# Performance work log

Measured on AMD Instinct MI355X. Metric: run time of the kernel, lower is better.

Reference implementation:

```python
import jax, jax.numpy as jnp
import numpy as np


def setup_inputs() -> dict:
    key = jax.random.key(0)
    k1, k2, k3 = jax.random.split(key, 3)
    B, C, H, W = 4, 256, 96, 128
    F = 9
    return {
        "input1": jax.random.normal(k1, (B, C, H, W), dtype=jnp.float32),
        "input2": jax.random.normal(k2, (B, C, H, W), dtype=jnp.float32),
        "weights": jax.random.normal(k3, (C, F, F), dtype=jnp.float32),
        "filter_size": 9,
        "dilation": 2,
        "num_groups": 4,
    }


def _weighted_corr(input1, input2, weights, filter_size, dilation, num_groups):
    B, C, H, W = input1.shape
    F = filter_size
    G = num_groups
    Cg = C // G
    r = F // 2
    pad = r * dilation
    # zero-pad input2 spatially so out-of-bounds displacements contribute 0
    p2 = jnp.pad(input2, ((0, 0), (0, 0), (pad, pad), (pad, pad)))
    in1g = input1.reshape(B, G, Cg, H, W)
    outs = []  # one [B, G, H, W] map per window offset (dy, dx)
    for dy in range(F):
        for dx in range(F):
            shifted = p2[:, :, dy * dilation:dy * dilation + H,
                         dx * dilation:dx * dilation + W].reshape(B, G, Cg, H, W)
            wg = weights[:, dy, dx].reshape(G, Cg)
            outs.append(jnp.einsum('bgchw,bgchw,gc->bghw', in1g, shifted, wg))
    out = jnp.stack(outs, axis=2)  # [B, G, F*F, H, W]
    return out.reshape(B, G * F * F, H, W)


def reference(input1, input2, weights, filter_size, dilation, num_groups):
    return _weighted_corr(input1, input2, weights, filter_size, dilation, num_groups)
```

## Files before the change

### kernel.cpp

```cpp
#include <hip/hip_runtime.h>

#define B_   4
#define C_   256
#define H_   96
#define W_   128
#define F_   9
#define G_   4
#define CG   64
#define NC4  16
#define NO   81
#define TH   2
#define TCOLS (W_ + 16)
#define HW_  (H_ * W_)

#define NDY   3
#define PROWS (2 * NDY)
#define PTE   (PROWS * TCOLS)
#define PNK   4

typedef _Float16 half2v __attribute__((ext_vector_type(2)));
typedef unsigned u32x2 __attribute__((ext_vector_type(2)));

__device__ __forceinline__ half2v u2h(unsigned u) {
    half2v h; __builtin_memcpy(&h, &u, 4); return h;
}
__device__ __forceinline__ unsigned h2u(half2v h) {
    unsigned u; __builtin_memcpy(&u, &h, 4); return u;
}
__device__ __forceinline__ half2v pkrtz(float a, float b) {
    auto r = __builtin_amdgcn_cvt_pkrtz(a, b);
    half2v h; __builtin_memcpy(&h, &r, 4); return h;
}
__device__ __forceinline__ unsigned pkrtz_u(float a, float b) {
    auto r = __builtin_amdgcn_cvt_pkrtz(a, b);
    unsigned u; __builtin_memcpy(&u, &r, 4); return u;
}

#if __has_builtin(__builtin_amdgcn_fdot2)
#define FDOT2(a, b, c) __builtin_amdgcn_fdot2((a), (b), (c), false)
#else
__device__ __forceinline__ float fdot2_fb(half2v a, half2v b, float c) {
    return c + (float)a[0] * (float)b[0] + (float)a[1] * (float)b[1];
}
#define FDOT2(a, b, c) fdot2_fb((a), (b), (c))
#endif

__global__ void pack_weights_kernel(const float* __restrict__ w,
                                    u32x2* __restrict__ wp) {
    int i = blockIdx.x * blockDim.x + threadIdx.x;
    if (i >= G_ * NC4 * NO) return;
    int o  = i % NO;
    int c4 = (i / NO) % NC4;
    int g  = i / (NO * NC4);
    const float* base = w + (size_t)(g * CG + 4 * c4) * NO + o;
    u32x2 r;
    r.x = pkrtz_u(base[0], base[NO]);
    r.y = pkrtz_u(base[2 * NO], base[3 * NO]);
    wp[i] = r;
}

template <bool PACKED>
__global__ __launch_bounds__(256)
void wcorr_kernel(const float* __restrict__ in1, const float* __restrict__ in2,
                  const u32x2* __restrict__ wp, const float* __restrict__ wraw,
                  float* __restrict__ out) {
    __shared__ u32x2 tile[2][PTE];

    int bid  = blockIdx.x;
    int xcd  = bid & 7;
    int slot = bid >> 3;
    int pair = xcd + 8 * (slot / 144);
    int rem  = slot % 144;
    int pass = rem / 48;
    int hblk = rem % 48;
    int b = pair >> 2, g = pair & 3;
    int h0 = hblk * TH;

    int t  = threadIdx.x;
    int ty = t >> 7;
    int tx = t & 127;

    const float* in1g = in1 + (size_t)(b * C_ + g * CG) * HW_;
    const float* in2g = in2 + (size_t)(b * C_ + g * CG) * HW_;

    const int gr0 = h0 - 8 + 6 * pass;
    int po[PNK]; unsigned msk[PNK];
#pragma unroll
    for (int k = 0; k < PNK; ++k) {
        int pidx = k * 256 + t;
        int row  = pidx / TCOLS;
        int hcol = pidx - row * TCOLS;
        int gr = gr0 + row, gc = hcol - 8;
        bool inb = (pidx < PTE) && gr >= 0 && gr < H_ && gc >= 0 && gc < W_;
        int off = gr * W_ + gc;
        off = off < 0 ? 0 : (off > HW_ - 1 ? HW_ - 1 : off);
        po[k]  = off;
        float m = inb ? 1.f : 0.f;
        msk[k] = pkrtz_u(m, m);
    }

    float acc[NDY * F_];
#pragma unroll
    for (int o = 0; o < NDY * F_; ++o) acc[o] = 0.f;

    float sv0[PNK], sv1[PNK], sv2[PNK], sv3[PNK];

    auto LOADS = [&](int c4n) {
        const float* chb = in2g + (size_t)(4 * c4n) * HW_;
#pragma unroll
        for (int k = 0; k < PNK; ++k) {
            const float* q = chb + po[k];
            sv0[k] = q[0];        sv1[k] = q[HW_];
            sv2[k] = q[2 * HW_];  sv3[k] = q[3 * HW_];
        }
    };
    auto WRITE = [&](u32x2* dst) {
#pragma unroll
        for (int k = 0; k < PNK; ++k) {
            if (k < PNK - 1 || t < PTE - (PNK - 1) * 256) {
                half2v m = u2h(msk[k]);
                u32x2 r;
                r.x = h2u(u2h(pkrtz_u(sv0[k], sv1[k])) * m);
                r.y = h2u(u2h(pkrtz_u(sv2[k], sv3[k])) * m);
                dst[k * 256 + t] = r;
            }
        }
    };

    LOADS(0);
    WRITE(tile[0]);
    LOADS(1);

    const int in1off = (h0 + ty) * W_ + tx;
    float a0 = in1g[in1off], a1 = in1g[in1off + HW_];
    float a2 = in1g[in1off + 2 * HW_], a3 = in1g[in1off + 3 * HW_];

    const int lbase = ty * TCOLS + tx;

    for (int c4 = 0; c4 < NC4; ++c4) {
        __syncthreads();

        if (c4 + 1 < NC4) WRITE(tile[(c4 + 1) & 1]);
        if (c4 + 2 < NC4) LOADS(c4 + 2);

        const u32x2* lt = tile[c4 & 1];
        half2v ha = pkrtz(a0, a1);
        half2v hb = pkrtz(a2, a3);
        if (c4 + 1 < NC4) {
            const float* pp = in1g + (size_t)(4 * (c4 + 1)) * HW_ + in1off;
            a0 = pp[0]; a1 = pp[HW_]; a2 = pp[2 * HW_]; a3 = pp[3 * HW_];
        }

        const u32x2* wrow = PACKED ? (wp + ((size_t)g * NC4 + c4) * NO + pass * NDY * F_) : nullptr;
        const float* wr = wraw + (size_t)(g * CG + 4 * c4) * NO + pass * NDY * F_;

#pragma unroll
        for (int dyp = 0; dyp < NDY; ++dyp) {
#pragma unroll
            for (int dx = 0; dx < F_; ++dx) {
                const int oo = dyp * F_ + dx;
                u32x2 uv = lt[lbase + dyp * 2 * TCOLS + dx * 2];
                half2v wa, wb;
                if (PACKED) {
                    u32x2 wv = wrow[oo];
                    wa = u2h(wv.x); wb = u2h(wv.y);
                } else {
                    wa = pkrtz(wr[oo], wr[oo + NO]);
                    wb = pkrtz(wr[oo + 2 * NO], wr[oo + 3 * NO]);
                }
                half2v p0 = wa * ha;
                half2v p1 = wb * hb;
                float s = FDOT2(p0, u2h(uv.x), acc[oo]);
                acc[oo]  = FDOT2(p1, u2h(uv.y), s);
            }
        }
    }

    size_t obase = (((size_t)pair * NO + pass * NDY * F_) * H_ + (h0 + ty)) * W_ + tx;
#pragma unroll
    for (int oo = 0; oo < NDY * F_; ++oo)
        out[obase + (size_t)oo * HW_] = acc[oo];
}

extern "C" void kernel_launch(void* const* d_in, const int* in_sizes, int n_in,
                              void* d_out, int out_size, void* d_ws, size_t ws_size,
                              hipStream_t stream) {
    const float* in1  = (const float*)d_in[0];
    const float* in2  = (const float*)d_in[1];
    const float* wraw = (const float*)d_in[2];
    float* out = (float*)d_out;

    const size_t wp_bytes = (size_t)G_ * NC4 * NO * 8;
    const int nblocks = 16 * 3 * (H_ / TH);

    if (ws_size >= wp_bytes) {
        u32x2* wp = (u32x2*)d_ws;
        int n = G_ * NC4 * NO;
        pack_weights_kernel<<<(n + 255) / 256, 256, 0, stream>>>(wraw, wp);
        wcorr_kernel<true><<<nblocks, 256, 0, stream>>>(in1, in2, wp, wraw, out);
    } else {
        wcorr_kernel<false><<<nblocks, 256, 0, stream>>>(in1, in2, nullptr, wraw, out);
    }
}
```

Baseline: 76.82 us.

## Switch to 4x64 spatial tiles and 8-channel half-packed LDS slabs

```diff
diff --git a/kernel.cpp b/kernel.cpp
--- a/kernel.cpp
+++ b/kernel.cpp
@@ -7,19 +7,18 @@
 #define F_   9
 #define G_   4
 #define CG   64
-#define NC4  16
+#define NC8  8
 #define NO   81
-#define TH   2
-#define TCOLS (W_ + 16)
 #define HW_  (H_ * W_)
 
 #define NDY   3
-#define PROWS (2 * NDY)
-#define PTE   (PROWS * TCOLS)
-#define PNK   4
+#define TROWS 8
+#define TCOLS 80
+#define PTE   (TROWS * TCOLS)
+#define PNK   3
 
 typedef _Float16 half2v __attribute__((ext_vector_type(2)));
-typedef unsigned u32x2 __attribute__((ext_vector_type(2)));
+typedef unsigned u32x4 __attribute__((ext_vector_type(4)));
 
 __device__ __forceinline__ half2v u2h(unsigned u) {
     half2v h; __builtin_memcpy(&h, &u, 4); return h;
@@ -46,25 +45,27 @@
 #endif
 
 __global__ void pack_weights_kernel(const float* __restrict__ w,
-                                    u32x2* __restrict__ wp) {
+                                    u32x4* __restrict__ wp) {
     int i = blockIdx.x * blockDim.x + threadIdx.x;
-    if (i >= G_ * NC4 * NO) return;
+    if (i >= G_ * NC8 * NO) return;
     int o  = i % NO;
-    int c4 = (i / NO) % NC4;
-    int g  = i / (NO * NC4);
-    const float* base = w + (size_t)(g * CG + 4 * c4) * NO + o;
-    u32x2 r;
-    r.x = pkrtz_u(base[0], base[NO]);
+    int c8 = (i / NO) % NC8;
+    int g  = i / (NO * NC8);
+    const float* base = w + (size_t)(g * CG + 8 * c8) * NO + o;
+    u32x4 r;
+    r.x = pkrtz_u(base[0 * NO], base[1 * NO]);
     r.y = pkrtz_u(base[2 * NO], base[3 * NO]);
+    r.z = pkrtz_u(base[4 * NO], base[5 * NO]);
+    r.w = pkrtz_u(base[6 * NO], base[7 * NO]);
     wp[i] = r;
 }
 
 template <bool PACKED>
 __global__ __launch_bounds__(256)
 void wcorr_kernel(const float* __restrict__ in1, const float* __restrict__ in2,
-                  const u32x2* __restrict__ wp, const float* __restrict__ wraw,
+                  const u32x4* __restrict__ wp, const float* __restrict__ wraw,
                   float* __restrict__ out) {
-    __shared__ u32x2 tile[2][PTE];
+    __shared__ u32x4 tile[2][PTE];
 
     int bid  = blockIdx.x;
     int xcd  = bid & 7;
@@ -72,25 +73,29 @@
     int pair = xcd + 8 * (slot / 144);
     int rem  = slot % 144;
     int pass = rem / 48;
-    int hblk = rem % 48;
+    int sub  = rem % 48;
+    int hblk = sub >> 1;
+    int half = sub & 1;
     int b = pair >> 2, g = pair & 3;
-    int h0 = hblk * TH;
-
-    int t  = threadIdx.x;
-    int ty = t >> 7;
-    int tx = t & 127;
+    int h0 = hblk * 4;
+    int w0 = half * 64;
+
+    int t = threadIdx.x;
+    int r = t >> 6;
+    int x = t & 63;
 
     const float* in1g = in1 + (size_t)(b * C_ + g * CG) * HW_;
     const float* in2g = in2 + (size_t)(b * C_ + g * CG) * HW_;
 
     const int gr0 = h0 - 8 + 6 * pass;
+    const int gc0 = w0 - 8;
     int po[PNK]; unsigned msk[PNK];
 #pragma unroll
     for (int k = 0; k < PNK; ++k) {
         int pidx = k * 256 + t;
         int row  = pidx / TCOLS;
-        int hcol = pidx - row * TCOLS;
-        int gr = gr0 + row, gc = hcol - 8;
+        int col  = pidx - row * TCOLS;
+        int gr = gr0 + row, gc = gc0 + col;
         bool inb = (pidx < PTE) && gr >= 0 && gr < H_ && gc >= 0 && gc < W_;
         int off = gr * W_ + gc;
         off = off < 0 ? 0 : (off > HW_ - 1 ? HW_ - 1 : off);
@@ -103,26 +108,28 @@
 #pragma unroll
     for (int o = 0; o < NDY * F_; ++o) acc[o] = 0.f;
 
-    float sv0[PNK], sv1[PNK], sv2[PNK], sv3[PNK];
-
-    auto LOADS = [&](int c4n) {
-        const float* chb = in2g + (size_t)(4 * c4n) * HW_;
+    float sv[PNK][8];
+
+    auto LOADS = [&](int c8n) {
+        const float* chb = in2g + (size_t)(8 * c8n) * HW_;
 #pragma unroll
         for (int k = 0; k < PNK; ++k) {
             const float* q = chb + po[k];
-            sv0[k] = q[0];        sv1[k] = q[HW_];
-            sv2[k] = q[2 * HW_];  sv3[k] = q[3 * HW_];
+#pragma unroll
+            for (int j = 0; j < 8; ++j) sv[k][j] = q[(size_t)j * HW_];
         }
     };
-    auto WRITE = [&](u32x2* dst) {
+    auto WRITE = [&](u32x4* dst) {
 #pragma unroll
         for (int k = 0; k < PNK; ++k) {
             if (k < PNK - 1 || t < PTE - (PNK - 1) * 256) {
                 half2v m = u2h(msk[k]);
-                u32x2 r;
-                r.x = h2u(u2h(pkrtz_u(sv0[k], sv1[k])) * m);
-                r.y = h2u(u2h(pkrtz_u(sv2[k], sv3[k])) * m);
-                dst[k * 256 + t] = r;
+                u32x4 e;
+                e.x = h2u(u2h(pkrtz_u(sv[k][0], sv[k][1])) * m);
+                e.y = h2u(u2h(pkrtz_u(sv[k][2], sv[k][3])) * m);
+                e.z = h2u(u2h(pkrtz_u(sv[k][4], sv[k][5])) * m);
+                e.w = h2u(u2h(pkrtz_u(sv[k][6], sv[k][7])) * m);
+                dst[k * 256 + t] = e;
             }
         }
     };
@@ -131,52 +138,58 @@
     WRITE(tile[0]);
     LOADS(1);
 
-    const int in1off = (h0 + ty) * W_ + tx;
-    float a0 = in1g[in1off], a1 = in1g[in1off + HW_];
-    float a2 = in1g[in1off + 2 * HW_], a3 = in1g[in1off + 3 * HW_];
-
-    const int lbase = ty * TCOLS + tx;
-
-    for (int c4 = 0; c4 < NC4; ++c4) {
+    const int in1off = (h0 + r) * W_ + (w0 + x);
+    float a[8];
+#pragma unroll
+    for (int j = 0; j < 8; ++j) a[j] = in1g[in1off + (size_t)j * HW_];
+
+    for (int c8 = 0; c8 < NC8; ++c8) {
         __syncthreads();
 
-        if (c4 + 1 < NC4) WRITE(tile[(c4 + 1) & 1]);
-        if (c4 + 2 < NC4) LOADS(c4 + 2);
-
-        const u32x2* lt = tile[c4 & 1];
-        half2v ha = pkrtz(a0, a1);
-        half2v hb = pkrtz(a2, a3);
-        if (c4 + 1 < NC4) {
-            const float* pp = in1g + (size_t)(4 * (c4 + 1)) * HW_ + in1off;
-            a0 = pp[0]; a1 = pp[HW_]; a2 = pp[2 * HW_]; a3 = pp[3 * HW_];
-        }
-
-        const u32x2* wrow = PACKED ? (wp + ((size_t)g * NC4 + c4) * NO + pass * NDY * F_) : nullptr;
-        const float* wr = wraw + (size_t)(g * CG + 4 * c4) * NO + pass * NDY * F_;
+        if (c8 + 1 < NC8) WRITE(tile[(c8 + 1) & 1]);
+        if (c8 + 2 < NC8) LOADS(c8 + 2);
+
+        half2v ha0 = pkrtz(a[0], a[1]), ha1 = pkrtz(a[2], a[3]);
+        half2v ha2 = pkrtz(a[4], a[5]), ha3 = pkrtz(a[6], a[7]);
+        if (c8 + 1 < NC8) {
+            const float* pp = in1g + (size_t)(8 * (c8 + 1)) * HW_ + in1off;
+#pragma unroll
+            for (int j = 0; j < 8; ++j) a[j] = pp[(size_t)j * HW_];
+        }
+
+        const u32x4* lt = tile[c8 & 1];
+        const u32x4* wrow = PACKED ? (wp + ((size_t)g * NC8 + c8) * NO + pass * NDY * F_) : nullptr;
+        const float* wr = wraw + (size_t)(g * CG + 8 * c8) * NO + pass * NDY * F_;
 
 #pragma unroll
         for (int dyp = 0; dyp < NDY; ++dyp) {
+            const u32x4* rowp = lt + (r + 2 * dyp) * TCOLS + x;
 #pragma unroll
             for (int dx = 0; dx < F_; ++dx) {
                 const int oo = dyp * F_ + dx;
-                u32x2 uv = lt[lbase + dyp * 2 * TCOLS + dx * 2];
-                half2v wa, wb;
+                u32x4 uv = rowp[2 * dx];
+                half2v w0h, w1h, w2h, w3h;
                 if (PACKED) {
-                    u32x2 wv = wrow[oo];
-                    wa = u2h(wv.x); wb = u2h(wv.y);
+                    u32x4 wv = wrow[oo];
+                    w0h = u2h(wv.x); w1h = u2h(wv.y);
+                    w2h = u2h(wv.z); w3h = u2h(wv.w);
                 } else {
-                    wa = pkrtz(wr[oo], wr[oo + NO]);
-                    wb = pkrtz(wr[oo + 2 * NO], wr[oo + 3 * NO]);
+                    w0h = pkrtz(wr[oo + 0 * NO], wr[oo + 1 * NO]);
+                    w1h = pkrtz(wr[oo + 2 * NO], wr[oo + 3 * NO]);
+                    w2h = pkrtz(wr[oo + 4 * NO], wr[oo + 5 * NO]);
+                    w3h = pkrtz(wr[oo + 6 * NO], wr[oo + 7 * NO]);
                 }
-                half2v p0 = wa * ha;
-                half2v p1 = wb * hb;
-                float s = FDOT2(p0, u2h(uv.x), acc[oo]);
-                acc[oo]  = FDOT2(p1, u2h(uv.y), s);
+                float s = acc[oo];
+                s = FDOT2(w0h * ha0, u2h(uv.x), s);
+                s = FDOT2(w1h * ha1, u2h(uv.y), s);
+                s = FDOT2(w2h * ha2, u2h(uv.z), s);
+                s = FDOT2(w3h * ha3, u2h(uv.w), s);
+                acc[oo] = s;
             }
         }
     }
 
-    size_t obase = (((size_t)pair * NO + pass * NDY * F_) * H_ + (h0 + ty)) * W_ + tx;
+    size_t obase = (((size_t)pair * NO + pass * NDY * F_) * H_ + (h0 + r)) * W_ + (w0 + x);
 #pragma unroll
     for (int oo = 0; oo < NDY * F_; ++oo)
         out[obase + (size_t)oo * HW_] = acc[oo];
@@ -190,12 +203,12 @@
     const float* wraw = (const float*)d_in[2];
     float* out = (float*)d_out;
 
-    const size_t wp_bytes = (size_t)G_ * NC4 * NO * 8;
-    const int nblocks = 16 * 3 * (H_ / TH);
+    const size_t wp_bytes = (size_t)G_ * NC8 * NO * 16;
+    const int nblocks = 16 * 144;
 
     if (ws_size >= wp_bytes) {
-        u32x2* wp = (u32x2*)d_ws;
-        int n = G_ * NC4 * NO;
+        u32x4* wp = (u32x4*)d_ws;
+        int n = G_ * NC8 * NO;
         pack_weights_kernel<<<(n + 255) / 256, 256, 0, stream>>>(wraw, wp);
         wcorr_kernel<true><<<nblocks, 256, 0, stream>>>(in1, in2, wp, wraw, out);
     } else {
```

Result: faster. 74.60 us (-2.9%).
